# Kernel tuning notes

Measured on AMD Instinct MI355X. Metric: run time of the kernel, lower is better.

Reference implementation:

```python
import jax, jax.numpy as jnp
import numpy as np

B, N, D, H = 128, 2000, 128, 8
HD = D // H  # head_dim = 16
CLIP = 10.0


def setup_inputs() -> dict:
    key = jax.random.key(0)
    ks = jax.random.split(key, 20)
    s = 0.05
    w = lambda k, sh: jax.random.normal(k, sh, jnp.float32) * s
    return {
        "embeddings": jax.random.normal(ks[0], (B, N, D), jnp.float32),
        "context": jax.random.normal(ks[1], (B, D), jnp.float32),
        "step_context": jax.random.normal(ks[2], (B, 1, D + 1), jnp.float32),
        "mask": jax.random.randint(ks[3], (B, 1, N), 0, 2).astype(bool),
        "Wq_c": w(ks[4], (D, D)), "bq_c": w(ks[5], (D,)),
        "Wq_s": w(ks[6], (D, D + 1)), "bq_s": w(ks[7], (D,)),
        "Wk": w(ks[8], (D, D)), "bk": w(ks[9], (D,)),
        "Wkt": w(ks[10], (D, D)), "bkt": w(ks[11], (D,)),
        "Wv": w(ks[12], (D, D)), "bv": w(ks[13], (D,)),
        "Wo": w(ks[14], (D, D)), "bo": w(ks[15], (D,)),
    }


def _heads(x):
    # (B, S, D) -> (B, H, S, HD)
    return x.reshape(x.shape[0], x.shape[1], H, HD).transpose(0, 2, 1, 3)


def reference(embeddings, context, step_context, mask,
              Wq_c, bq_c, Wq_s, bq_s, Wk, bk, Wkt, bkt, Wv, bv, Wo, bo):
    # get_projections
    K = _heads(embeddings @ Wk.T + bk)        # (B, H, N, HD)
    V = _heads(embeddings @ Wv.T + bv)        # (B, H, N, HD)
    K_tanh = embeddings @ Wkt.T + bkt         # (B, N, D)
    Q_context = context[:, None, :] @ Wq_c.T + bq_c     # (B, 1, D)
    Q_step = step_context @ Wq_s.T + bq_s                # (B, 1, D)
    Q = _heads(Q_context + Q_step)            # (B, H, 1, HD)

    # decoder_mha: matmul -> mask(-inf) -> softmax -> mask(0) -> matmul -> w_out
    compat = jnp.einsum('bhqd,bhkd->bhqk', Q, K) / jnp.sqrt(jnp.float32(HD))
    m4 = mask[:, None, :, :]                  # (B, 1, 1, N) broadcast over heads
    compat = jnp.where(m4, -jnp.inf, compat)
    attn_w = jax.nn.softmax(compat, axis=-1)
    attn_w = jnp.where(m4, 0.0, attn_w)
    attn = jnp.einsum('bhqk,bhkd->bhqd', attn_w, V)      # (B, H, 1, HD)
    mha = attn.transpose(0, 2, 1, 3).reshape(B, -1, D) @ Wo.T + bo  # (B, 1, D)

    # get_log_p: matmul -> mask(-inf) -> log_softmax
    # NOTE: the original computes tanh(compat)*clip into `x` but never uses it
    # (dead code) -- replicated faithfully by omitting the clip.
    logits = jnp.einsum('bqd,bkd->bqk', mha, K_tanh) / jnp.sqrt(jnp.float32(D))
    logits = jnp.where(mask, -jnp.inf, logits)
    return jax.nn.log_softmax(logits, axis=-1)  # (B, 1, N)
```

## Files before the change

### kernel.cpp

```cpp
#include <hip/hip_runtime.h>
#include <cstdint>
#include <cstddef>
#include <math.h>

#define B 128
#define N 2000
#define D 128
#define H 8
#define HD 16
#define NCA 8
#define TPCA 250
#define NCL 16
#define TPCL 125
#define NEG_BIG (-1.0e30f)

#define DOT4(e, w) ((e).x*(w).x + (e).y*(w).y + (e).z*(w).z + (e).w*(w).w)

__global__ __launch_bounds__(128) void k_prep(
    const float* __restrict__ ctx, const float* __restrict__ sctx,
    const float* __restrict__ Wq_c, const float* __restrict__ bq_c,
    const float* __restrict__ Wq_s, const float* __restrict__ bq_s,
    const float* __restrict__ Wk,   const float* __restrict__ bk,
    float* __restrict__ wq, float* __restrict__ cq)
{
    int b = blockIdx.x, t = threadIdx.x;
    __shared__ float4 c14[D / 4];
    __shared__ float c2s[D + 1], Qs[D];
    if (t < D / 4) c14[t] = reinterpret_cast<const float4*>(ctx + b * D)[t];
    c2s[t] = sctx[b * (D + 1) + t];
    if (t == 0) c2s[D] = sctx[b * (D + 1) + D];
    __syncthreads();
    float q = bq_c[t] + bq_s[t];
    const float4* wc4 = reinterpret_cast<const float4*>(Wq_c + t * D);
    #pragma unroll 8
    for (int j = 0; j < D / 4; j++) {
        float4 w = wc4[j], c = c14[j];
        q += w.x * c.x + w.y * c.y + w.z * c.z + w.w * c.w;
    }
    const float* wsr = Wq_s + t * (D + 1);
    #pragma unroll 8
    for (int j = 0; j < D + 1; j++) q += wsr[j] * c2s[j];
    Qs[t] = q;
    __syncthreads();
    float acc[H] = {};
    #pragma unroll
    for (int r = 0; r < D; r++)
        acc[r >> 4] += Wk[r * D + t] * Qs[r];
    #pragma unroll
    for (int h = 0; h < H; h++) wq[b * (H * D) + h * D + t] = acc[h] * 0.25f;
    if (t < H) {
        float c = 0.f;
        #pragma unroll
        for (int i = 0; i < HD; i++) c += Qs[t * HD + i] * bk[t * HD + i];
        cq[b * H + t] = c * 0.25f;
    }
}

__global__ __launch_bounds__(256, 4) void k_attn(
    const float* __restrict__ emb, const unsigned char* __restrict__ mask,
    const float* __restrict__ wq, const float* __restrict__ cq,
    float* __restrict__ pl, float* __restrict__ ps)
{
    int b = blockIdx.y, c = blockIdx.x, t = threadIdx.x;
    int n0 = c * TPCA;
    int wave = t >> 6;

    __shared__ __align__(16) float shmem[4096];
    __shared__ float cqs_s[H];
    __shared__ float redl[4][H];

    float4* wqs   = reinterpret_cast<float4*>(shmem);
    float4* plds4 = reinterpret_cast<float4*>(shmem + 1024);

    wqs[t] = reinterpret_cast<const float4*>(wq + b * (H * D))[t];
    if (t < H) cqs_s[t] = cq[b * H + t];
    __syncthreads();

    const float4* e4 = reinterpret_cast<const float4*>(emb + (size_t)b * N * D);

    {
        int qtok = t >> 2, qp = t & 3;
        int r3 = qtok + 192 < TPCA ? qtok + 192 : 0;
        const float4* er0 = e4 + (size_t)(n0 + qtok      ) * 32;
        const float4* er1 = e4 + (size_t)(n0 + qtok +  64) * 32;
        const float4* er2 = e4 + (size_t)(n0 + qtok + 128) * 32;
        const float4* er3 = e4 + (size_t)(n0 + r3        ) * 32;
        float a0[H] = {}, a1[H] = {}, a2[H] = {}, a3[H] = {};
        #pragma unroll
        for (int j = 0; j < 8; j++) {
            int o = j * 4 + qp;
            float4 e0 = er0[o], e1 = er1[o], e2 = er2[o], e3 = er3[o];
            #pragma unroll
            for (int h = 0; h < H; h++) {
                float4 w = wqs[h * 32 + o];
                a0[h] += DOT4(e0, w); a1[h] += DOT4(e1, w);
                a2[h] += DOT4(e2, w); a3[h] += DOT4(e3, w);
            }
        }
        #pragma unroll
        for (int h = 0; h < H; h++) {
            a0[h] += __shfl_xor(a0[h], 1); a0[h] += __shfl_xor(a0[h], 2);
            a1[h] += __shfl_xor(a1[h], 1); a1[h] += __shfl_xor(a1[h], 2);
            a2[h] += __shfl_xor(a2[h], 1); a2[h] += __shfl_xor(a2[h], 2);
            a3[h] += __shfl_xor(a3[h], 1); a3[h] += __shfl_xor(a3[h], 2);
        }
        if (qp == 0) {
            const unsigned char* mrow = mask + (size_t)b * N + n0;
            bool d0 = mrow[qtok] != 0;
            bool d1 = mrow[qtok + 64] != 0;
            bool d2 = mrow[qtok + 128] != 0;
            bool d3 = (qtok + 192 >= TPCA) || (mrow[r3] != 0);
            float4 pa, pb;
            #define EMIT(ACC, DEAD, TOK) \
                pa.x = (DEAD) ? 0.f : __expf(ACC[0] + cqs_s[0]); \
                pa.y = (DEAD) ? 0.f : __expf(ACC[1] + cqs_s[1]); \
                pa.z = (DEAD) ? 0.f : __expf(ACC[2] + cqs_s[2]); \
                pa.w = (DEAD) ? 0.f : __expf(ACC[3] + cqs_s[3]); \
                pb.x = (DEAD) ? 0.f : __expf(ACC[4] + cqs_s[4]); \
                pb.y = (DEAD) ? 0.f : __expf(ACC[5] + cqs_s[5]); \
                pb.z = (DEAD) ? 0.f : __expf(ACC[6] + cqs_s[6]); \
                pb.w = (DEAD) ? 0.f : __expf(ACC[7] + cqs_s[7]); \
                plds4[(TOK) * 3] = pa; plds4[(TOK) * 3 + 1] = pb;
            EMIT(a0, d0, qtok)
            EMIT(a1, d1, qtok + 64)
            EMIT(a2, d2, qtok + 128)
            if (qtok + 192 < TPCA) { EMIT(a3, d3, qtok + 192) }
            #undef EMIT
        }
    }
    __syncthreads();

    int grp = t >> 5, gl = t & 31;
    float4 a[H];
    float  La[H];
    #pragma unroll
    for (int h = 0; h < H; h++) { a[h] = {0.f, 0.f, 0.f, 0.f}; La[h] = 0.f; }
    for (int i = grp; i < TPCA; i += 8) {
        float4 pA = plds4[i * 3];
        float4 pB = plds4[i * 3 + 1];
        float4 e = e4[(size_t)(n0 + i) * 32 + gl];
        a[0].x += pA.x * e.x; a[0].y += pA.x * e.y; a[0].z += pA.x * e.z; a[0].w += pA.x * e.w;
        a[1].x += pA.y * e.x; a[1].y += pA.y * e.y; a[1].z += pA.y * e.z; a[1].w += pA.y * e.w;
        a[2].x += pA.z * e.x; a[2].y += pA.z * e.y; a[2].z += pA.z * e.z; a[2].w += pA.z * e.w;
        a[3].x += pA.w * e.x; a[3].y += pA.w * e.y; a[3].z += pA.w * e.z; a[3].w += pA.w * e.w;
        a[4].x += pB.x * e.x; a[4].y += pB.x * e.y; a[4].z += pB.x * e.z; a[4].w += pB.x * e.w;
        a[5].x += pB.y * e.x; a[5].y += pB.y * e.y; a[5].z += pB.y * e.z; a[5].w += pB.y * e.w;
        a[6].x += pB.z * e.x; a[6].y += pB.z * e.y; a[6].z += pB.z * e.z; a[6].w += pB.z * e.w;
        a[7].x += pB.w * e.x; a[7].y += pB.w * e.y; a[7].z += pB.w * e.z; a[7].w += pB.w * e.w;
        La[0] += pA.x; La[1] += pA.y; La[2] += pA.z; La[3] += pA.w;
        La[4] += pB.x; La[5] += pB.y; La[6] += pB.z; La[7] += pB.w;
    }
    __syncthreads();

    #pragma unroll
    for (int h = 0; h < H; h++) {
        a[h].x += __shfl_xor(a[h].x, 32);
        a[h].y += __shfl_xor(a[h].y, 32);
        a[h].z += __shfl_xor(a[h].z, 32);
        a[h].w += __shfl_xor(a[h].w, 32);
        La[h]  += __shfl_xor(La[h], 32);
    }
    float4* reds = reinterpret_cast<float4*>(shmem);
    if ((t & 32) == 0) {
        #pragma unroll
        for (int h = 0; h < H; h++) reds[(wave * H + h) * 32 + gl] = a[h];
    }
    if ((t & 63) == 0) {
        #pragma unroll
        for (int h = 0; h < H; h++) redl[wave][h] = La[h];
    }
    __syncthreads();

    {
        int hh = t >> 5, dd = gl;
        float4 r = reds[(0 * H + hh) * 32 + dd];
        #pragma unroll
        for (int w2 = 1; w2 < 4; w2++) {
            float4 x = reds[(w2 * H + hh) * 32 + dd];
            r.x += x.x; r.y += x.y; r.z += x.z; r.w += x.w;
        }
        reinterpret_cast<float4*>(ps + (((size_t)(b * NCA + c)) * H + hh) * D)[dd] = r;
        if (t < H)
            pl[(b * NCA + c) * H + t] = redl[0][t] + redl[1][t] + redl[2][t] + redl[3][t];
    }
}

__global__ __launch_bounds__(128) void k_comb(
    const float* __restrict__ pl, const float* __restrict__ ps,
    const float* __restrict__ Wv, const float* __restrict__ bv,
    const float* __restrict__ Wo, const float* __restrict__ bo,
    const float* __restrict__ Wkt, const float* __restrict__ bkt,
    float* __restrict__ g, float* __restrict__ c2)
{
    int b = blockIdx.x, t = threadIdx.x;
    __shared__ float invLs[H];
    __shared__ float s_s[H][D + 4];
    __shared__ float attn_s[D];
    __shared__ float mha_s[D];
    if (t < H) {
        float L = 0.f;
        #pragma unroll
        for (int c = 0; c < NCA; c++) L += pl[(b * NCA + c) * H + t];
        invLs[t] = 1.0f / L;
    }
    __syncthreads();
    #pragma unroll
    for (int h = 0; h < H; h++) {
        float v = 0.f;
        #pragma unroll
        for (int c = 0; c < NCA; c++)
            v += ps[(((size_t)(b * NCA + c)) * H + h) * D + t];
        s_s[h][t] = v * invLs[h];
    }
    __syncthreads();
    {
        int h = t >> 4;
        const float* wr = Wv + t * D;
        float a = bv[t];
        #pragma unroll 8
        for (int d = 0; d < D; d++) a += wr[d] * s_s[h][d];
        attn_s[t] = a;
    }
    __syncthreads();
    {
        const float* wr = Wo + t * D;
        float m = bo[t];
        #pragma unroll 8
        for (int r = 0; r < D; r++) m += wr[r] * attn_s[r];
        mha_s[t] = m;
    }
    __syncthreads();
    {
        float gv = 0.f;
        #pragma unroll 8
        for (int d = 0; d < D; d++) gv += Wkt[d * D + t] * mha_s[d];
        g[b * D + t] = gv * 0.08838834764831845f;
    }
    if (t == 0) {
        float c = 0.f;
        #pragma unroll 8
        for (int d = 0; d < D; d++) c += mha_s[d] * bkt[d];
        c2[b] = c * 0.08838834764831845f;
    }
}

__global__ __launch_bounds__(256) void k_logits(
    const float* __restrict__ emb, const unsigned char* __restrict__ mask,
    const float* __restrict__ g, const float* __restrict__ c2,
    float* __restrict__ out)
{
    int b = blockIdx.y, t = threadIdx.x;
    int qtok = t >> 2, qp = t & 3;
    __shared__ float4 gs[D / 4];
    __shared__ float c2s;
    if (t < D / 4) gs[t] = reinterpret_cast<const float4*>(g + b * D)[t];
    if (t == 0) c2s = c2[b];
    __syncthreads();
    int n0 = blockIdx.x * TPCL;
    const float4* e4 = reinterpret_cast<const float4*>(emb + (size_t)b * N * D);
    #pragma unroll
    for (int k = 0; k < 2; k++) {
        int ng = k * 64 + qtok;
        bool live = (ng < TPCL);
        int nr = live ? (n0 + ng) : n0;
        const float4* erow = e4 + (size_t)nr * 32;
        float acc = 0.f;
        #pragma unroll
        for (int j = 0; j < 8; j++) {
            float4 e = erow[j * 4 + qp];
            float4 w = gs[j * 4 + qp];
            acc += e.x * w.x + e.y * w.y + e.z * w.z + e.w * w.w;
        }
        acc += __shfl_xor(acc, 1);
        acc += __shfl_xor(acc, 2);
        if (live && qp == 0) {
            bool m = mask[(size_t)b * N + nr] != 0;
            out[(size_t)b * N + nr] = m ? -INFINITY : (acc + c2s);
        }
    }
}

__global__ __launch_bounds__(256) void k_lsm(float* __restrict__ out)
{
    __shared__ float red[4];
    int t = threadIdx.x;
    float* row = out + (size_t)blockIdx.x * N;
    float v[8];
    float mx = -INFINITY;
    #pragma unroll
    for (int i = 0; i < 8; i++) {
        int idx = t + i * 256;
        v[i] = (idx < N) ? row[idx] : -INFINITY;
        mx = fmaxf(mx, v[i]);
    }
    #pragma unroll
    for (int o = 32; o; o >>= 1) mx = fmaxf(mx, __shfl_xor(mx, o));
    if ((t & 63) == 0) red[t >> 6] = mx;
    __syncthreads();
    mx = fmaxf(fmaxf(red[0], red[1]), fmaxf(red[2], red[3]));
    __syncthreads();
    float s = 0.f;
    #pragma unroll
    for (int i = 0; i < 8; i++)
        if (v[i] != -INFINITY) s += __expf(v[i] - mx);
    #pragma unroll
    for (int o = 32; o; o >>= 1) s += __shfl_xor(s, o);
    if ((t & 63) == 0) red[t >> 6] = s;
    __syncthreads();
    s = red[0] + red[1] + red[2] + red[3];
    float lse = mx + logf(s);
    #pragma unroll
    for (int i = 0; i < 8; i++) {
        int idx = t + i * 256;
        if (idx < N) row[idx] = (v[i] == -INFINITY) ? NEG_BIG : (v[i] - lse);
    }
}

extern "C" void kernel_launch(void* const* d_in, const int* in_sizes, int n_in,
                              void* d_out, int out_size, void* d_ws, size_t ws_size,
                              hipStream_t stream)
{
    const float* emb  = (const float*)d_in[0];
    const float* ctx  = (const float*)d_in[1];
    const float* sctx = (const float*)d_in[2];
    const unsigned char* mask = (const unsigned char*)d_in[3];
    const float* Wq_c = (const float*)d_in[4];
    const float* bq_c = (const float*)d_in[5];
    const float* Wq_s = (const float*)d_in[6];
    const float* bq_s = (const float*)d_in[7];
    const float* Wk   = (const float*)d_in[8];
    const float* bk   = (const float*)d_in[9];
    const float* Wkt  = (const float*)d_in[10];
    const float* bkt  = (const float*)d_in[11];
    const float* Wv   = (const float*)d_in[12];
    const float* bv   = (const float*)d_in[13];
    const float* Wo   = (const float*)d_in[14];
    const float* bo   = (const float*)d_in[15];
    float* out = (float*)d_out;

    float* ws = (float*)d_ws;
    float* wq = ws;
    float* cq = ws + 131072;
    float* pl = ws + 132096;
    float* ps = ws + 140288;
    float* g  = ws + 1188864;
    float* c2 = ws + 1205248;

    k_prep  <<<dim3(B), dim3(128), 0, stream>>>(ctx, sctx, Wq_c, bq_c, Wq_s, bq_s, Wk, bk, wq, cq);
    k_attn  <<<dim3(NCA, B), dim3(256), 0, stream>>>(emb, mask, wq, cq, pl, ps);
    k_comb  <<<dim3(B), dim3(128), 0, stream>>>(pl, ps, Wv, bv, Wo, bo, Wkt, bkt, g, c2);
    k_logits<<<dim3(NCL, B), dim3(256), 0, stream>>>(emb, mask, g, c2, out);
    k_lsm   <<<dim3(B), dim3(256), 0, stream>>>(out);
}
```

Measured before the change: 102.4 us.

## Split attention into 16 chunks per batch and split heads across thread groups

Doubles the number of attention blocks per batch row by halving the tokens per chunk, and raises the launch-bounds occupancy hint. The weighted-sum phase now has each 32-thread group handle half the heads, which cuts per-thread accumulator registers, and the reduction is rewritten to match. The aim is more parallelism and higher occupancy for the memory-bound embedding pass. In exchange the partial-sum buffer doubles in size, so the combine kernel reads more partials. It relies on k_comb already looping over NCA.

```diff
diff --git a/kernel.cpp b/kernel.cpp
--- a/kernel.cpp
+++ b/kernel.cpp
@@ -8,8 +8,8 @@
 #define D 128
 #define H 8
 #define HD 16
-#define NCA 8
-#define TPCA 250
+#define NCA 16
+#define TPCA 125
 #define NCL 16
 #define TPCL 125
 #define NEG_BIG (-1.0e30f)
@@ -56,18 +56,17 @@
     }
 }
 
-__global__ __launch_bounds__(256, 4) void k_attn(
+__global__ __launch_bounds__(256, 8) void k_attn(
     const float* __restrict__ emb, const unsigned char* __restrict__ mask,
     const float* __restrict__ wq, const float* __restrict__ cq,
     float* __restrict__ pl, float* __restrict__ ps)
 {
     int b = blockIdx.y, c = blockIdx.x, t = threadIdx.x;
     int n0 = c * TPCA;
-    int wave = t >> 6;
 
     __shared__ __align__(16) float shmem[4096];
     __shared__ float cqs_s[H];
-    __shared__ float redl[4][H];
+    __shared__ float redl[8][4];
 
     float4* wqs   = reinterpret_cast<float4*>(shmem);
     float4* plds4 = reinterpret_cast<float4*>(shmem + 1024);
@@ -80,36 +79,31 @@
 
     {
         int qtok = t >> 2, qp = t & 3;
-        int r3 = qtok + 192 < TPCA ? qtok + 192 : 0;
-        const float4* er0 = e4 + (size_t)(n0 + qtok      ) * 32;
-        const float4* er1 = e4 + (size_t)(n0 + qtok +  64) * 32;
-        const float4* er2 = e4 + (size_t)(n0 + qtok + 128) * 32;
-        const float4* er3 = e4 + (size_t)(n0 + r3        ) * 32;
-        float a0[H] = {}, a1[H] = {}, a2[H] = {}, a3[H] = {};
+        bool live1 = (qtok + 64 < TPCA);
+        int r1 = live1 ? (qtok + 64) : 0;
+        const float4* er0 = e4 + (size_t)(n0 + qtok) * 32;
+        const float4* er1 = e4 + (size_t)(n0 + r1) * 32;
+        float a0[H] = {}, a1[H] = {};
         #pragma unroll
         for (int j = 0; j < 8; j++) {
             int o = j * 4 + qp;
-            float4 e0 = er0[o], e1 = er1[o], e2 = er2[o], e3 = er3[o];
+            float4 e0 = er0[o], e1 = er1[o];
             #pragma unroll
             for (int h = 0; h < H; h++) {
                 float4 w = wqs[h * 32 + o];
-                a0[h] += DOT4(e0, w); a1[h] += DOT4(e1, w);
-                a2[h] += DOT4(e2, w); a3[h] += DOT4(e3, w);
+                a0[h] += DOT4(e0, w);
+                a1[h] += DOT4(e1, w);
             }
         }
         #pragma unroll
         for (int h = 0; h < H; h++) {
             a0[h] += __shfl_xor(a0[h], 1); a0[h] += __shfl_xor(a0[h], 2);
             a1[h] += __shfl_xor(a1[h], 1); a1[h] += __shfl_xor(a1[h], 2);
-            a2[h] += __shfl_xor(a2[h], 1); a2[h] += __shfl_xor(a2[h], 2);
-            a3[h] += __shfl_xor(a3[h], 1); a3[h] += __shfl_xor(a3[h], 2);
         }
         if (qp == 0) {
             const unsigned char* mrow = mask + (size_t)b * N + n0;
             bool d0 = mrow[qtok] != 0;
-            bool d1 = mrow[qtok + 64] != 0;
-            bool d2 = mrow[qtok + 128] != 0;
-            bool d3 = (qtok + 192 >= TPCA) || (mrow[r3] != 0);
+            bool d1 = !live1 || (mrow[r1] != 0);
             float4 pa, pb;
             #define EMIT(ACC, DEAD, TOK) \
                 pa.x = (DEAD) ? 0.f : __expf(ACC[0] + cqs_s[0]); \
@@ -122,66 +116,56 @@
                 pb.w = (DEAD) ? 0.f : __expf(ACC[7] + cqs_s[7]); \
                 plds4[(TOK) * 3] = pa; plds4[(TOK) * 3 + 1] = pb;
             EMIT(a0, d0, qtok)
-            EMIT(a1, d1, qtok + 64)
-            EMIT(a2, d2, qtok + 128)
-            if (qtok + 192 < TPCA) { EMIT(a3, d3, qtok + 192) }
+            if (live1) { EMIT(a1, d1, qtok + 64) }
             #undef EMIT
         }
     }
     __syncthreads();
 
     int grp = t >> 5, gl = t & 31;
-    float4 a[H];
-    float  La[H];
-    #pragma unroll
-    for (int h = 0; h < H; h++) { a[h] = {0.f, 0.f, 0.f, 0.f}; La[h] = 0.f; }
-    for (int i = grp; i < TPCA; i += 8) {
-        float4 pA = plds4[i * 3];
-        float4 pB = plds4[i * 3 + 1];
+    int half = grp & 1;
+    int tset = grp >> 1;
+    float4 a[4];
+    float  La[4];
+    #pragma unroll
+    for (int h = 0; h < 4; h++) { a[h] = {0.f, 0.f, 0.f, 0.f}; La[h] = 0.f; }
+    for (int i = tset; i < TPCA; i += 4) {
+        float4 p = plds4[i * 3 + half];
         float4 e = e4[(size_t)(n0 + i) * 32 + gl];
-        a[0].x += pA.x * e.x; a[0].y += pA.x * e.y; a[0].z += pA.x * e.z; a[0].w += pA.x * e.w;
-        a[1].x += pA.y * e.x; a[1].y += pA.y * e.y; a[1].z += pA.y * e.z; a[1].w += pA.y * e.w;
-        a[2].x += pA.z * e.x; a[2].y += pA.z * e.y; a[2].z += pA.z * e.z; a[2].w += pA.z * e.w;
-        a[3].x += pA.w * e.x; a[3].y += pA.w * e.y; a[3].z += pA.w * e.z; a[3].w += pA.w * e.w;
-        a[4].x += pB.x * e.x; a[4].y += pB.x * e.y; a[4].z += pB.x * e.z; a[4].w += pB.x * e.w;
-        a[5].x += pB.y * e.x; a[5].y += pB.y * e.y; a[5].z += pB.y * e.z; a[5].w += pB.y * e.w;
-        a[6].x += pB.z * e.x; a[6].y += pB.z * e.y; a[6].z += pB.z * e.z; a[6].w += pB.z * e.w;
-        a[7].x += pB.w * e.x; a[7].y += pB.w * e.y; a[7].z += pB.w * e.z; a[7].w += pB.w * e.w;
-        La[0] += pA.x; La[1] += pA.y; La[2] += pA.z; La[3] += pA.w;
-        La[4] += pB.x; La[5] += pB.y; La[6] += pB.z; La[7] += pB.w;
-    }
-    __syncthreads();
-
-    #pragma unroll
-    for (int h = 0; h < H; h++) {
-        a[h].x += __shfl_xor(a[h].x, 32);
-        a[h].y += __shfl_xor(a[h].y, 32);
-        a[h].z += __shfl_xor(a[h].z, 32);
-        a[h].w += __shfl_xor(a[h].w, 32);
-        La[h]  += __shfl_xor(La[h], 32);
-    }
+        a[0].x += p.x * e.x; a[0].y += p.x * e.y; a[0].z += p.x * e.z; a[0].w += p.x * e.w;
+        a[1].x += p.y * e.x; a[1].y += p.y * e.y; a[1].z += p.y * e.z; a[1].w += p.y * e.w;
+        a[2].x += p.z * e.x; a[2].y += p.z * e.y; a[2].z += p.z * e.z; a[2].w += p.z * e.w;
+        a[3].x += p.w * e.x; a[3].y += p.w * e.y; a[3].z += p.w * e.z; a[3].w += p.w * e.w;
+        La[0] += p.x; La[1] += p.y; La[2] += p.z; La[3] += p.w;
+    }
+    __syncthreads();
+
     float4* reds = reinterpret_cast<float4*>(shmem);
-    if ((t & 32) == 0) {
-        #pragma unroll
-        for (int h = 0; h < H; h++) reds[(wave * H + h) * 32 + gl] = a[h];
-    }
-    if ((t & 63) == 0) {
-        #pragma unroll
-        for (int h = 0; h < H; h++) redl[wave][h] = La[h];
+    #pragma unroll
+    for (int h = 0; h < 4; h++) reds[(grp * 4 + h) * 32 + gl] = a[h];
+    if (gl == 0) {
+        #pragma unroll
+        for (int h = 0; h < 4; h++) redl[grp][h] = La[h];
     }
     __syncthreads();
 
     {
         int hh = t >> 5, dd = gl;
-        float4 r = reds[(0 * H + hh) * 32 + dd];
-        #pragma unroll
-        for (int w2 = 1; w2 < 4; w2++) {
-            float4 x = reds[(w2 * H + hh) * 32 + dd];
+        int hf = hh >> 2, hl = hh & 3;
+        float4 r = {0.f, 0.f, 0.f, 0.f};
+        #pragma unroll
+        for (int ts = 0; ts < 4; ts++) {
+            float4 x = reds[((ts * 2 + hf) * 4 + hl) * 32 + dd];
             r.x += x.x; r.y += x.y; r.z += x.z; r.w += x.w;
         }
         reinterpret_cast<float4*>(ps + (((size_t)(b * NCA + c)) * H + hh) * D)[dd] = r;
-        if (t < H)
-            pl[(b * NCA + c) * H + t] = redl[0][t] + redl[1][t] + redl[2][t] + redl[3][t];
+        if (t < H) {
+            int hf2 = t >> 2, hl2 = t & 3;
+            float L = 0.f;
+            #pragma unroll
+            for (int ts = 0; ts < 4; ts++) L += redl[ts * 2 + hf2][hl2];
+            pl[(b * NCA + c) * H + t] = L;
+        }
     }
 }
 
@@ -342,9 +326,9 @@
     float* wq = ws;
     float* cq = ws + 131072;
     float* pl = ws + 132096;
-    float* ps = ws + 140288;
-    float* g  = ws + 1188864;
-    float* c2 = ws + 1205248;
+    float* ps = ws + 148480;
+    float* g  = ws + 2245632;
+    float* c2 = ws + 2262016;
 
     k_prep  <<<dim3(B), dim3(128), 0, stream>>>(ctx, sctx, Wq_c, bq_c, Wq_s, bq_s, Wk, bk, wq, cq);
     k_attn  <<<dim3(NCA, B), dim3(256), 0, stream>>>(emb, mask, wq, cq, pl, ps);
```

New measurement: 98.60 us. 3.7% less time.
